# Optimization experiments

Hardware: AMD Instinct MI355X
Metric: run time of the kernel (lower is better)

## Reference

```python
import jax, jax.numpy as jnp
import numpy as np

DIM_Q = 512
DIM_K = 512
D_Q4 = float(DIM_Q) ** 0.25  # torch: dim_q ** (1/4)
D_K4 = float(DIM_K) ** 0.25


def setup_inputs() -> dict:
    key = jax.random.key(0)
    ks = jax.random.split(key, 9)
    B, N, D_IN = 8, 4096, 512
    s_in = 1.0 / np.sqrt(D_IN)
    return {
        "x_q": jax.random.normal(ks[0], (B, N, D_IN), jnp.float32),
        "x_k": jax.random.normal(ks[1], (B, N, D_IN), jnp.float32),
        "x_v": jax.random.normal(ks[2], (B, N, D_IN), jnp.float32),
        # Linear params stored as [in, out] for x @ W + b
        "W_q": jax.random.uniform(ks[3], (D_IN, DIM_Q), jnp.float32, -s_in, s_in),
        "b_q": jax.random.uniform(ks[4], (DIM_Q,), jnp.float32, -s_in, s_in),
        "W_k": jax.random.uniform(ks[5], (D_IN, DIM_K), jnp.float32, -s_in, s_in),
        "b_k": jax.random.uniform(ks[6], (DIM_K,), jnp.float32, -s_in, s_in),
        "W_v": jax.random.uniform(ks[7], (D_IN, DIM_K), jnp.float32, -s_in, s_in),
        "b_v": jax.random.uniform(ks[8], (DIM_K,), jnp.float32, -s_in, s_in),
    }


def reference(x_q, x_k, x_v, W_q, b_q, W_k, b_k, W_v, b_v):
    Q = x_q @ W_q + b_q          # [B, n, dq]
    K = x_k @ W_k + b_k          # [B, n, dk]
    V = x_v @ W_v + b_v          # [B, n, dk]
    # softmax_row: over sequence axis (dim=-2) of Q
    A = jax.nn.softmax(Q / D_Q4, axis=-2)          # [B, n, dq]
    # softmax_col on K^T (dim=-1) == softmax over sequence axis of K
    Ks = jax.nn.softmax(K / D_K4, axis=-2)         # [B, n, dk]
    Bm = jnp.einsum("bnd,bne->bde", Ks, V)        # [B, dk, dk]
    Z = jnp.einsum("bnd,bde->bne", A, Bm)         # [B, n, dk]
    return Z
```

## Files before the change

### kernel.cpp

```cpp
#include <hip/hip_runtime.h>
#include <hip/hip_bf16.h>


typedef __bf16 bf16_t;
typedef __attribute__((ext_vector_type(8))) __bf16 bf16x8;
typedef __attribute__((ext_vector_type(4))) __bf16 bf16x4;
typedef __attribute__((ext_vector_type(4))) float f32x4;

#define MFMA_BF16 __builtin_amdgcn_mfma_f32_16x16x32_bf16

__device__ inline void async_ld16(const void* g, void* l) {
  __builtin_amdgcn_global_load_lds(
      (const __attribute__((address_space(1))) void*)g,
      (__attribute__((address_space(3))) void*)l, 16, 0, 0);
}

#define INV_D4 0.2102241038134287f

#define BAR_LGKM()                                        \
  do {                                                    \
    asm volatile("s_waitcnt lgkmcnt(0)" ::: "memory");    \
    __builtin_amdgcn_s_barrier();                         \
  } while (0)

#define BAR_VM_LGKM()                                             \
  do {                                                            \
    asm volatile("s_waitcnt vmcnt(0) lgkmcnt(0)" ::: "memory");   \
    __builtin_amdgcn_s_barrier();                                 \
  } while (0)

__device__ inline void cvt_store4(bf16_t* dst, const float4* f, int cch,
                                  int xr, int half) {
#pragma unroll
  for (int i = 0; i < 4; ++i) {
    bf16x4 v;
    v[0] = (__bf16)f[i].x; v[1] = (__bf16)f[i].y;
    v[2] = (__bf16)f[i].z; v[3] = (__bf16)f[i].w;
    *(bf16x4*)(dst + (size_t)(cch * 132 + xr + 32 * i) * 8 + half * 4) = v;
  }
}

__global__ __launch_bounds__(256) void wt_kernel(
    const float* __restrict__ Wq, const float* __restrict__ Wk,
    const float* __restrict__ Wv, bf16_t* __restrict__ Wt) {
  const int z = blockIdx.z;
  const float* W = (z == 0) ? Wq : (z == 1) ? Wk : Wv;
  bf16_t* O = Wt + (size_t)z * 262144;
  __shared__ __align__(16) bf16_t tile[64 * 72];
  const int t = threadIdx.x;
  const int r = t >> 2;
  const int c4 = (t & 3) * 16;
  const int in0 = blockIdx.x * 64, out0 = blockIdx.y * 64;
  const float* src = W + (size_t)(in0 + r) * 512 + out0 + c4;
#pragma unroll
  for (int i = 0; i < 4; ++i) {
    float4 f = ((const float4*)src)[i];
    tile[(c4 + i * 4 + 0) * 72 + r] = (__bf16)f.x;
    tile[(c4 + i * 4 + 1) * 72 + r] = (__bf16)f.y;
    tile[(c4 + i * 4 + 2) * 72 + r] = (__bf16)f.z;
    tile[(c4 + i * 4 + 3) * 72 + r] = (__bf16)f.w;
  }
  __syncthreads();
  bf16x8* dst = (bf16x8*)(O + (size_t)(out0 + r) * 512 + in0 + c4);
  const bf16x8* s = (const bf16x8*)(tile + r * 72 + c4);
  dst[0] = s[0];
  dst[1] = s[1];
}

__global__ __launch_bounds__(256, 2) void proj_q(
    const float* __restrict__ Xq, const bf16_t* __restrict__ Wt,
    const float* __restrict__ bias, bf16_t* __restrict__ Eq,
    float* __restrict__ Sq) {
  __shared__ __align__(16) bf16_t Xs[2][4224];

  const int t = threadIdx.x;
  const int lane = t & 63, w = t >> 6;
  const int quad = lane >> 4, l15 = lane & 15;
  const int m0 = blockIdx.x * 128;
  const int n0 = blockIdx.y * 256 + w * 64;

  f32x4 acc[8][4];
  const f32x4 zero4 = {0.f, 0.f, 0.f, 0.f};
#pragma unroll
  for (int i = 0; i < 8; ++i)
#pragma unroll
    for (int j = 0; j < 4; ++j) acc[i][j] = zero4;

  const int xr = t >> 3;
  const int f4 = t & 7;
  const int cch = f4 >> 1, half = f4 & 1;
  const float* abase = Xq + (size_t)(m0 + xr) * 512 + f4 * 4;
  const bf16_t* wbase = Wt + (size_t)(n0 + l15) * 512 + quad * 8;

  float4 fb[2][4];
  bf16x8 wr[2][4];

#pragma unroll
  for (int i = 0; i < 4; ++i) fb[1][i] = *(const float4*)(abase + i * 16384);
#pragma unroll
  for (int ni = 0; ni < 4; ++ni)
    wr[0][ni] = *(const bf16x8*)(wbase + ni * 8192);
#pragma unroll
  for (int i = 0; i < 4; ++i)
    fb[0][i] = *(const float4*)(abase + i * 16384 + 32);
  cvt_store4(Xs[0], fb[1], cch, xr, half);
#pragma unroll
  for (int i = 0; i < 4; ++i)
    fb[1][i] = *(const float4*)(abase + i * 16384 + 64);
  BAR_LGKM();

#pragma unroll
  for (int ks = 0; ks < 16; ++ks) {
    const int p = ks & 1;
    bf16x8 af[8];
#pragma unroll
    for (int mi = 0; mi < 8; ++mi)
      af[mi] = *(const bf16x8*)(&Xs[p][(size_t)(quad * 132 + mi * 16 + l15) * 8]);
    if (ks < 15) {
      cvt_store4(Xs[p ^ 1], fb[p], cch, xr, half);
#pragma unroll
      for (int ni = 0; ni < 4; ++ni)
        wr[p ^ 1][ni] = *(const bf16x8*)(wbase + ni * 8192 + (ks + 1) * 32);
      if (ks < 13) {
#pragma unroll
        for (int i = 0; i < 4; ++i)
          fb[p][i] = *(const float4*)(abase + i * 16384 + (ks + 3) * 32);
      }
    }
#pragma unroll
    for (int mi = 0; mi < 8; ++mi)
#pragma unroll
      for (int ni = 0; ni < 4; ++ni)
        acc[mi][ni] = MFMA_BF16(af[mi], wr[p][ni], acc[mi][ni], 0, 0, 0);
    if (ks < 15) BAR_LGKM();
  }

  const int b = m0 >> 12;
  float cs[4] = {0.f, 0.f, 0.f, 0.f};
#pragma unroll
  for (int ni = 0; ni < 4; ++ni) {
    const int col = n0 + ni * 16 + l15;
    const float bv_ = bias[col];
#pragma unroll
    for (int mi = 0; mi < 8; ++mi)
#pragma unroll
      for (int r = 0; r < 4; ++r) {
        const int row = m0 + mi * 16 + quad * 4 + r;
        float v = __expf((acc[mi][ni][r] + bv_) * INV_D4);
        Eq[(size_t)row * 512 + col] = (bf16_t)v;
        cs[ni] += v;
      }
  }
#pragma unroll
  for (int ni = 0; ni < 4; ++ni) {
    cs[ni] += __shfl_xor(cs[ni], 16);
    cs[ni] += __shfl_xor(cs[ni], 32);
  }
  if (lane < 16) {
#pragma unroll
    for (int ni = 0; ni < 4; ++ni)
      atomicAdd(&Sq[b * 512 + n0 + ni * 16 + lane], cs[ni]);
  }
}

__global__ __launch_bounds__(256, 2) void proj_kv(
    const float* __restrict__ xk, const float* __restrict__ xv,
    const bf16_t* __restrict__ Wt, const float* __restrict__ bk,
    const float* __restrict__ bv, bf16_t* __restrict__ Ft,
    bf16_t* __restrict__ Vt) {
  const int z = blockIdx.z + 1;
  const float* X = (z == 1) ? xk : xv;
  const float* bias = (z == 1) ? bk : bv;
  const bf16_t* W = Wt + (size_t)z * 262144;
  bf16_t* Out = (z == 1) ? Ft : Vt;
  const bool expm = (z == 1);

  __shared__ __align__(16) bf16_t Xs[2][4224];

  const int t = threadIdx.x;
  const int lane = t & 63, w = t >> 6;
  const int quad = lane >> 4, l15 = lane & 15;
  const int ng = blockIdx.x * 128;
  const int d0 = blockIdx.y * 256 + w * 64;

  f32x4 acc[4][8];
  const f32x4 zero4 = {0.f, 0.f, 0.f, 0.f};
#pragma unroll
  for (int i = 0; i < 4; ++i)
#pragma unroll
    for (int j = 0; j < 8; ++j) acc[i][j] = zero4;

  const int xr = t >> 3;
  const int f4 = t & 7;
  const int cch = f4 >> 1, half = f4 & 1;
  const float* bbase = X + (size_t)(ng + xr) * 512 + f4 * 4;
  const bf16_t* wbase = W + (size_t)(d0 + l15) * 512 + quad * 8;

  float4 fb[2][4];
  bf16x8 wr[2][4];

#pragma unroll
  for (int i = 0; i < 4; ++i) fb[1][i] = *(const float4*)(bbase + i * 16384);
#pragma unroll
  for (int mi = 0; mi < 4; ++mi)
    wr[0][mi] = *(const bf16x8*)(wbase + mi * 8192);
#pragma unroll
  for (int i = 0; i < 4; ++i)
    fb[0][i] = *(const float4*)(bbase + i * 16384 + 32);
  cvt_store4(Xs[0], fb[1], cch, xr, half);
#pragma unroll
  for (int i = 0; i < 4; ++i)
    fb[1][i] = *(const float4*)(bbase + i * 16384 + 64);
  BAR_LGKM();

#pragma unroll
  for (int ks = 0; ks < 16; ++ks) {
    const int p = ks & 1;
    bf16x8 bx[8];
#pragma unroll
    for (int ni = 0; ni < 8; ++ni)
      bx[ni] = *(const bf16x8*)(&Xs[p][(size_t)(quad * 132 + ni * 16 + l15) * 8]);
    if (ks < 15) {
      cvt_store4(Xs[p ^ 1], fb[p], cch, xr, half);
#pragma unroll
      for (int mi = 0; mi < 4; ++mi)
        wr[p ^ 1][mi] = *(const bf16x8*)(wbase + mi * 8192 + (ks + 1) * 32);
      if (ks < 13) {
#pragma unroll
        for (int i = 0; i < 4; ++i)
          fb[p][i] = *(const float4*)(bbase + i * 16384 + (ks + 3) * 32);
      }
    }
#pragma unroll
    for (int mi = 0; mi < 4; ++mi)
#pragma unroll
      for (int ni = 0; ni < 8; ++ni)
        acc[mi][ni] = MFMA_BF16(wr[p][mi], bx[ni], acc[mi][ni], 0, 0, 0);
    if (ks < 15) BAR_LGKM();
  }

  const int b = ng >> 12;
  const int nl0 = (ng & 4095);
#pragma unroll
  for (int mi = 0; mi < 4; ++mi)
#pragma unroll
    for (int r = 0; r < 4; ++r) {
      const int d = d0 + mi * 16 + quad * 4 + r;
      const float bv_ = bias[d];
      bf16_t* rowp = Out + (size_t)b * 2097152 + (size_t)d * 4096 + nl0;
#pragma unroll
      for (int ni = 0; ni < 8; ++ni) {
        float v = acc[mi][ni][r] + bv_;
        if (expm) v = __expf(v * INV_D4);
        rowp[ni * 16 + l15] = (bf16_t)v;
      }
    }
}

__global__ __launch_bounds__(256) void sk_kernel(const bf16_t* __restrict__ Ft,
                                                 float* __restrict__ Sk) {
  const int row = blockIdx.x * 4 + (threadIdx.x >> 6);
  const int lane = threadIdx.x & 63;
  const bf16x8* p = (const bf16x8*)(Ft + (size_t)row * 4096) + lane;
  float s = 0.f;
#pragma unroll
  for (int j = 0; j < 8; ++j) {
    bf16x8 v = p[j * 64];
#pragma unroll
    for (int e = 0; e < 8; ++e) s += (float)v[e];
  }
#pragma unroll
  for (int m = 1; m <= 32; m <<= 1) s += __shfl_xor(s, m);
  if (lane == 0) Sk[row] = s;
}

__global__ __launch_bounds__(256, 2) void bm_gemm(
    const bf16_t* __restrict__ Ft, const bf16_t* __restrict__ Vt,
    float* __restrict__ Bmp, int S) {
  const int b = blockIdx.z / S;
  const int s = blockIdx.z - b * S;
  const int d0 = blockIdx.x * 128;
  const int e0 = blockIdx.y * 128;
  const bf16_t* A = Ft + (size_t)b * 2097152;
  const bf16_t* B = Vt + (size_t)b * 2097152;
  float* out = Bmp + ((size_t)s * 8 + b) * 262144;

  __shared__ __align__(16) bf16_t As[2][8192];
  __shared__ __align__(16) bf16_t Bs[2][8192];

  const int t = threadIdx.x;
  const int lane = t & 63, w = t >> 6;
  const int quad = lane >> 4, l15 = lane & 15;
  const int m_off = (w & 1) * 64, n_off = (w >> 1) * 64;

  const int kper = 4096 / S;
  const int KS = kper >> 6;
  const int kbase = s * kper;

  f32x4 acc[4][4];
  const f32x4 zero4 = {0.f, 0.f, 0.f, 0.f};
#pragma unroll
  for (int i = 0; i < 4; ++i)
#pragma unroll
    for (int j = 0; j < 4; ++j) acc[i][j] = zero4;

  const int srow = lane >> 3;
  const int spiece = (lane & 7) ^ srow;
  const bf16_t* asrc = A + (size_t)(d0 + srow) * 4096 + kbase + spiece * 8;
  const bf16_t* bsrc = B + (size_t)(e0 + srow) * 4096 + kbase + spiece * 8;
  const int q0 = w * 4;
  const int rsw = l15 & 7;

  auto stage = [&](int buf, int ks) {
#pragma unroll
    for (int i = 0; i < 4; ++i) {
      const int q = q0 + i;
      async_ld16(asrc + (size_t)q * 8 * 4096 + ks * 64, &As[buf][q * 512]);
      async_ld16(bsrc + (size_t)q * 8 * 4096 + ks * 64, &Bs[buf][q * 512]);
    }
  };

  stage(0, 0);
  BAR_VM_LGKM();

  for (int ks = 0; ks < KS; ++ks) {
    const int p = ks & 1;
    if (ks + 1 < KS) stage(p ^ 1, ks + 1);
#pragma unroll
    for (int ksub = 0; ksub < 2; ++ksub) {
      const int c = ksub * 4 + quad;
      bf16x8 af[4], bfr[4];
#pragma unroll
      for (int mi = 0; mi < 4; ++mi) {
        const int row = m_off + mi * 16 + l15;
        af[mi] = *(const bf16x8*)(&As[p][(size_t)row * 64 + ((c ^ rsw) << 3)]);
      }
#pragma unroll
      for (int ni = 0; ni < 4; ++ni) {
        const int row = n_off + ni * 16 + l15;
        bfr[ni] = *(const bf16x8*)(&Bs[p][(size_t)row * 64 + ((c ^ rsw) << 3)]);
      }
#pragma unroll
      for (int mi = 0; mi < 4; ++mi)
#pragma unroll
        for (int ni = 0; ni < 4; ++ni)
          acc[mi][ni] = MFMA_BF16(af[mi], bfr[ni], acc[mi][ni], 0, 0, 0);
    }
    if (ks + 1 < KS) BAR_VM_LGKM();
  }

#pragma unroll
  for (int mi = 0; mi < 4; ++mi)
#pragma unroll
    for (int ni = 0; ni < 4; ++ni) {
      const int ecol = e0 + n_off + ni * 16 + l15;
#pragma unroll
      for (int r = 0; r < 4; ++r) {
        const int drow = d0 + m_off + mi * 16 + quad * 4 + r;
        out[(size_t)drow * 512 + ecol] = acc[mi][ni][r];
      }
    }
}

__global__ __launch_bounds__(256) void scale_kernel(
    const float* __restrict__ Bmp, const float* __restrict__ Sq,
    const float* __restrict__ Sk, bf16_t* __restrict__ Ct, int S) {
  const int b = blockIdx.z;
  const int d0 = blockIdx.x * 64, e0 = blockIdx.y * 64;
  __shared__ __align__(16) bf16_t tile[64 * 72];
  const int t = threadIdx.x;
  const int r = t >> 2;
  const int c4 = (t & 3) * 16;
  const int d = d0 + r;
  const float f = 1.0f / (Sq[b * 512 + d] * Sk[b * 512 + d]);
  const float* p0 = Bmp + (size_t)b * 262144 + (size_t)d * 512 + e0 + c4;
#pragma unroll
  for (int i = 0; i < 4; ++i) {
    float sx = 0.f, sy = 0.f, sz = 0.f, sw = 0.f;
    for (int sp = 0; sp < S; ++sp) {
      float4 v = ((const float4*)(p0 + (size_t)sp * 2097152))[i];
      sx += v.x; sy += v.y; sz += v.z; sw += v.w;
    }
    tile[(c4 + i * 4 + 0) * 72 + r] = (__bf16)(sx * f);
    tile[(c4 + i * 4 + 1) * 72 + r] = (__bf16)(sy * f);
    tile[(c4 + i * 4 + 2) * 72 + r] = (__bf16)(sz * f);
    tile[(c4 + i * 4 + 3) * 72 + r] = (__bf16)(sw * f);
  }
  __syncthreads();
  bf16x8* dst = (bf16x8*)(Ct + (size_t)b * 262144 + (size_t)(e0 + r) * 512 + d0 + c4);
  const bf16x8* sptr = (const bf16x8*)(tile + r * 72 + c4);
  dst[0] = sptr[0];
  dst[1] = sptr[1];
}

__global__ __launch_bounds__(256, 2) void z_gemm(
    const bf16_t* __restrict__ Eq, const bf16_t* __restrict__ Ct,
    float* __restrict__ out) {
  __shared__ __align__(16) bf16_t As[2][8192];

  const int t = threadIdx.x;
  const int lane = t & 63, w = t >> 6;
  const int quad = lane >> 4, l15 = lane & 15;
  const int m0 = blockIdx.x * 128;
  const int n0 = blockIdx.y * 256 + w * 64;
  const int batch = m0 >> 12;
  const bf16_t* Bt = Ct + (size_t)batch * 262144;

  f32x4 acc[8][4];
  const f32x4 zero4 = {0.f, 0.f, 0.f, 0.f};
#pragma unroll
  for (int i = 0; i < 8; ++i)
#pragma unroll
    for (int j = 0; j < 4; ++j) acc[i][j] = zero4;

  const int srow = lane >> 3;
  const int spiece = (lane & 7) ^ srow;
  const bf16_t* asrc = Eq + (size_t)(m0 + srow) * 512 + spiece * 8;
  const int q0 = w * 4;
  const int rsw = l15 & 7;
  const bf16_t* wbase = Bt + (size_t)(n0 + l15) * 512 + quad * 8;

  auto stageZ = [&](int buf, int ks) {
#pragma unroll
    for (int i = 0; i < 4; ++i) {
      const int q = q0 + i;
      async_ld16(asrc + (size_t)q * 8 * 512 + ks * 64, &As[buf][q * 512]);
    }
  };

  stageZ(0, 0);
  BAR_VM_LGKM();

#pragma unroll
  for (int ks = 0; ks < 8; ++ks) {
    const int p = ks & 1;
    if (ks < 7) stageZ(p ^ 1, ks + 1);
    bf16x8 wrA[4], wrB[4];
#pragma unroll
    for (int ni = 0; ni < 4; ++ni) {
      wrA[ni] = *(const bf16x8*)(wbase + ni * 8192 + ks * 64);
      wrB[ni] = *(const bf16x8*)(wbase + ni * 8192 + ks * 64 + 32);
    }
#pragma unroll
    for (int ksub = 0; ksub < 2; ++ksub) {
      const int c = ksub * 4 + quad;
      bf16x8 af[8];
#pragma unroll
      for (int mi = 0; mi < 8; ++mi) {
        const int row = mi * 16 + l15;
        af[mi] = *(const bf16x8*)(&As[p][(size_t)row * 64 + ((c ^ rsw) << 3)]);
      }
#pragma unroll
      for (int mi = 0; mi < 8; ++mi)
#pragma unroll
        for (int ni = 0; ni < 4; ++ni)
          acc[mi][ni] =
              MFMA_BF16(af[mi], ksub ? wrB[ni] : wrA[ni], acc[mi][ni], 0, 0, 0);
    }
    if (ks < 7) BAR_VM_LGKM();
  }

#pragma unroll
  for (int mi = 0; mi < 8; ++mi)
#pragma unroll
    for (int ni = 0; ni < 4; ++ni) {
      const int col = n0 + ni * 16 + l15;
#pragma unroll
      for (int r = 0; r < 4; ++r) {
        const int row = m0 + mi * 16 + quad * 4 + r;
        out[(size_t)row * 512 + col] = acc[mi][ni][r];
      }
    }
}

extern "C" void kernel_launch(void* const* d_in, const int* in_sizes, int n_in,
                              void* d_out, int out_size, void* d_ws,
                              size_t ws_size, hipStream_t stream) {
  const float* xq = (const float*)d_in[0];
  const float* xk = (const float*)d_in[1];
  const float* xv = (const float*)d_in[2];
  const float* Wq = (const float*)d_in[3];
  const float* bq = (const float*)d_in[4];
  const float* Wk = (const float*)d_in[5];
  const float* bk = (const float*)d_in[6];
  const float* Wv = (const float*)d_in[7];
  const float* bv = (const float*)d_in[8];
  float* out = (float*)d_out;

  char* ws = (char*)d_ws;
  bf16_t* Eq = (bf16_t*)(ws + 0);
  bf16_t* Ft = (bf16_t*)(ws + 33554432);
  bf16_t* Vt = (bf16_t*)(ws + 67108864);
  float* Bmp = (float*)(ws + 100663296);

  const int S = (ws_size >= (size_t)135823360) ? 4 : 2;
  const size_t wt_off = (S == 4) ? (size_t)134217728 : (size_t)117440512;
  bf16_t* Wt = (bf16_t*)(ws + wt_off);
  float* Sq = (float*)(ws + wt_off + 1572864);
  float* Sk = (float*)(ws + wt_off + 1572864 + 16384);
  bf16_t* Ct = (bf16_t*)(ws + 33554432);

  hipMemsetAsync(Sq, 0, 16384, stream);

  wt_kernel<<<dim3(8, 8, 3), 256, 0, stream>>>(Wq, Wk, Wv, Wt);
  proj_q<<<dim3(256, 2), 256, 0, stream>>>(xq, Wt, bq, Eq, Sq);
  proj_kv<<<dim3(256, 2, 2), 256, 0, stream>>>(xk, xv, Wt, bk, bv, Ft, Vt);
  sk_kernel<<<dim3(1024), 256, 0, stream>>>(Ft, Sk);
  bm_gemm<<<dim3(4, 4, 8 * S), 256, 0, stream>>>(Ft, Vt, Bmp, S);
  scale_kernel<<<dim3(8, 8, 8), 256, 0, stream>>>(Bmp, Sq, Sk, Ct, S);
  z_gemm<<<dim3(256, 2), 256, 0, stream>>>(Eq, Ct, out);
}
```

Before: 357.2 us.

## Stage fp32 X tiles via async global-to-LDS loads with swizzle in projections

```diff
diff --git a/kernel.cpp b/kernel.cpp
--- a/kernel.cpp
+++ b/kernel.cpp
@@ -16,12 +16,6 @@
 }
 
 #define INV_D4 0.2102241038134287f
-
-#define BAR_LGKM()                                        \
-  do {                                                    \
-    asm volatile("s_waitcnt lgkmcnt(0)" ::: "memory");    \
-    __builtin_amdgcn_s_barrier();                         \
-  } while (0)
 
 #define BAR_VM_LGKM()                                             \
   do {                                                            \
@@ -29,15 +23,29 @@
     __builtin_amdgcn_s_barrier();                                 \
   } while (0)
 
-__device__ inline void cvt_store4(bf16_t* dst, const float4* f, int cch,
-                                  int xr, int half) {
-#pragma unroll
-  for (int i = 0; i < 4; ++i) {
-    bf16x4 v;
-    v[0] = (__bf16)f[i].x; v[1] = (__bf16)f[i].y;
-    v[2] = (__bf16)f[i].z; v[3] = (__bf16)f[i].w;
-    *(bf16x4*)(dst + (size_t)(cch * 132 + xr + 32 * i) * 8 + half * 4) = v;
-  }
+#define BAR_VM8_LGKM()                                            \
+  do {                                                            \
+    asm volatile("s_waitcnt vmcnt(8) lgkmcnt(0)" ::: "memory");   \
+    __builtin_amdgcn_s_barrier();                                 \
+  } while (0)
+
+#define STAGE_X(LBUF, KS)                                                  \
+  _Pragma("unroll") for (int i_ = 0; i_ < 8; ++i_) {                       \
+    const int rw_ = w * 32 + i_ * 4 + (lane >> 4);                         \
+    const int pc_ = (lane & 15) ^ (rw_ & 15);                              \
+    async_ld16(Xb + (size_t)rw_ * 512 + (KS) * 64 + pc_ * 4,               \
+               (char*)(LBUF) + (w * 32 + i_ * 4) * 256);                   \
+  }
+
+__device__ inline bf16x8 frag_cvt(const float* lbuf, int row, int p0) {
+  const char* base = (const char*)lbuf + row * 256;
+  const int s = row & 15;
+  f32x4 a = *(const f32x4*)(base + (((p0 + 0) ^ s) << 4));
+  f32x4 b = *(const f32x4*)(base + (((p0 + 1) ^ s) << 4));
+  bf16x8 r;
+  r[0] = (__bf16)a[0]; r[1] = (__bf16)a[1]; r[2] = (__bf16)a[2]; r[3] = (__bf16)a[3];
+  r[4] = (__bf16)b[0]; r[5] = (__bf16)b[1]; r[6] = (__bf16)b[2]; r[7] = (__bf16)b[3];
+  return r;
 }
 
 __global__ __launch_bounds__(256) void wt_kernel(
@@ -71,81 +79,74 @@
     const float* __restrict__ Xq, const bf16_t* __restrict__ Wt,
     const float* __restrict__ bias, bf16_t* __restrict__ Eq,
     float* __restrict__ Sq) {
-  __shared__ __align__(16) bf16_t Xs[2][4224];
+  __shared__ __align__(16) float Xf[2][8192];
 
   const int t = threadIdx.x;
   const int lane = t & 63, w = t >> 6;
   const int quad = lane >> 4, l15 = lane & 15;
   const int m0 = blockIdx.x * 128;
-  const int n0 = blockIdx.y * 256 + w * 64;
-
-  f32x4 acc[8][4];
+  const int n0 = blockIdx.y * 128;
+  const int m_off = (w & 1) * 64, n_off = (w >> 1) * 64;
+
+  f32x4 acc[4][4];
   const f32x4 zero4 = {0.f, 0.f, 0.f, 0.f};
 #pragma unroll
-  for (int i = 0; i < 8; ++i)
+  for (int i = 0; i < 4; ++i)
 #pragma unroll
     for (int j = 0; j < 4; ++j) acc[i][j] = zero4;
 
-  const int xr = t >> 3;
-  const int f4 = t & 7;
-  const int cch = f4 >> 1, half = f4 & 1;
-  const float* abase = Xq + (size_t)(m0 + xr) * 512 + f4 * 4;
-  const bf16_t* wbase = Wt + (size_t)(n0 + l15) * 512 + quad * 8;
-
-  float4 fb[2][4];
-  bf16x8 wr[2][4];
-
-#pragma unroll
-  for (int i = 0; i < 4; ++i) fb[1][i] = *(const float4*)(abase + i * 16384);
-#pragma unroll
-  for (int ni = 0; ni < 4; ++ni)
-    wr[0][ni] = *(const bf16x8*)(wbase + ni * 8192);
-#pragma unroll
-  for (int i = 0; i < 4; ++i)
-    fb[0][i] = *(const float4*)(abase + i * 16384 + 32);
-  cvt_store4(Xs[0], fb[1], cch, xr, half);
-#pragma unroll
-  for (int i = 0; i < 4; ++i)
-    fb[1][i] = *(const float4*)(abase + i * 16384 + 64);
-  BAR_LGKM();
-
-#pragma unroll
-  for (int ks = 0; ks < 16; ++ks) {
-    const int p = ks & 1;
-    bf16x8 af[8];
-#pragma unroll
-    for (int mi = 0; mi < 8; ++mi)
-      af[mi] = *(const bf16x8*)(&Xs[p][(size_t)(quad * 132 + mi * 16 + l15) * 8]);
-    if (ks < 15) {
-      cvt_store4(Xs[p ^ 1], fb[p], cch, xr, half);
-#pragma unroll
-      for (int ni = 0; ni < 4; ++ni)
-        wr[p ^ 1][ni] = *(const bf16x8*)(wbase + ni * 8192 + (ks + 1) * 32);
-      if (ks < 13) {
-#pragma unroll
-        for (int i = 0; i < 4; ++i)
-          fb[p][i] = *(const float4*)(abase + i * 16384 + (ks + 3) * 32);
-      }
-    }
-#pragma unroll
-    for (int mi = 0; mi < 8; ++mi)
-#pragma unroll
-      for (int ni = 0; ni < 4; ++ni)
-        acc[mi][ni] = MFMA_BF16(af[mi], wr[p][ni], acc[mi][ni], 0, 0, 0);
-    if (ks < 15) BAR_LGKM();
-  }
+  const float* Xb = Xq + (size_t)m0 * 512;
+  const bf16_t* wbase = Wt + (size_t)(n0 + n_off + l15) * 512 + quad * 8;
+
+  bf16x8 wA[4][2], wB[4][2];
+
+#define Q_LOAD_W(WBUF, KS)                                                 \
+  _Pragma("unroll") for (int ni_ = 0; ni_ < 4; ++ni_)                      \
+    _Pragma("unroll") for (int u_ = 0; u_ < 2; ++u_)                       \
+      WBUF[ni_][u_] =                                                      \
+          *(const bf16x8*)(wbase + ni_ * 8192 + (KS) * 64 + u_ * 32);
+
+#define Q_STEP(KS, CUR, NXT, WC, WN, FULL)                                 \
+  {                                                                        \
+    if (FULL) {                                                            \
+      STAGE_X(NXT, (KS) + 1);                                              \
+      asm volatile("" ::: "memory");                                       \
+      Q_LOAD_W(WN, (KS) + 1);                                              \
+    }                                                                      \
+    _Pragma("unroll") for (int u = 0; u < 2; ++u)                          \
+      _Pragma("unroll") for (int mi = 0; mi < 4; ++mi) {                   \
+        bf16x8 ax = frag_cvt(CUR, m_off + mi * 16 + l15, u * 8 + quad * 2);\
+        _Pragma("unroll") for (int ni = 0; ni < 4; ++ni)                   \
+          acc[mi][ni] = MFMA_BF16(ax, WC[ni][u], acc[mi][ni], 0, 0, 0);    \
+      }                                                                    \
+    if (FULL) BAR_VM8_LGKM();                                              \
+  }
+
+  STAGE_X(Xf[0], 0);
+  asm volatile("" ::: "memory");
+  Q_LOAD_W(wA, 0);
+  BAR_VM8_LGKM();
+
+  Q_STEP(0, Xf[0], Xf[1], wA, wB, true);
+  Q_STEP(1, Xf[1], Xf[0], wB, wA, true);
+  Q_STEP(2, Xf[0], Xf[1], wA, wB, true);
+  Q_STEP(3, Xf[1], Xf[0], wB, wA, true);
+  Q_STEP(4, Xf[0], Xf[1], wA, wB, true);
+  Q_STEP(5, Xf[1], Xf[0], wB, wA, true);
+  Q_STEP(6, Xf[0], Xf[1], wA, wB, true);
+  Q_STEP(7, Xf[1], Xf[0], wB, wA, false);
 
   const int b = m0 >> 12;
   float cs[4] = {0.f, 0.f, 0.f, 0.f};
 #pragma unroll
   for (int ni = 0; ni < 4; ++ni) {
-    const int col = n0 + ni * 16 + l15;
+    const int col = n0 + n_off + ni * 16 + l15;
     const float bv_ = bias[col];
 #pragma unroll
-    for (int mi = 0; mi < 8; ++mi)
+    for (int mi = 0; mi < 4; ++mi)
 #pragma unroll
       for (int r = 0; r < 4; ++r) {
-        const int row = m0 + mi * 16 + quad * 4 + r;
+        const int row = m0 + m_off + mi * 16 + quad * 4 + r;
         float v = __expf((acc[mi][ni][r] + bv_) * INV_D4);
         Eq[(size_t)row * 512 + col] = (bf16_t)v;
         cs[ni] += v;
@@ -159,8 +160,10 @@
   if (lane < 16) {
 #pragma unroll
     for (int ni = 0; ni < 4; ++ni)
-      atomicAdd(&Sq[b * 512 + n0 + ni * 16 + lane], cs[ni]);
-  }
+      atomicAdd(&Sq[b * 512 + n0 + n_off + ni * 16 + lane], cs[ni]);
+  }
+#undef Q_STEP
+#undef Q_LOAD_W
 }
 
 __global__ __launch_bounds__(256, 2) void proj_kv(
@@ -175,86 +178,81 @@
   bf16_t* Out = (z == 1) ? Ft : Vt;
   const bool expm = (z == 1);
 
-  __shared__ __align__(16) bf16_t Xs[2][4224];
+  __shared__ __align__(16) float Xf[2][8192];
 
   const int t = threadIdx.x;
   const int lane = t & 63, w = t >> 6;
   const int quad = lane >> 4, l15 = lane & 15;
   const int ng = blockIdx.x * 128;
-  const int d0 = blockIdx.y * 256 + w * 64;
-
-  f32x4 acc[4][8];
+  const int d0 = blockIdx.y * 128;
+  const int d_off = (w & 1) * 64, n_off = (w >> 1) * 64;
+
+  f32x4 acc[4][4];
   const f32x4 zero4 = {0.f, 0.f, 0.f, 0.f};
 #pragma unroll
   for (int i = 0; i < 4; ++i)
 #pragma unroll
-    for (int j = 0; j < 8; ++j) acc[i][j] = zero4;
-
-  const int xr = t >> 3;
-  const int f4 = t & 7;
-  const int cch = f4 >> 1, half = f4 & 1;
-  const float* bbase = X + (size_t)(ng + xr) * 512 + f4 * 4;
-  const bf16_t* wbase = W + (size_t)(d0 + l15) * 512 + quad * 8;
-
-  float4 fb[2][4];
-  bf16x8 wr[2][4];
-
-#pragma unroll
-  for (int i = 0; i < 4; ++i) fb[1][i] = *(const float4*)(bbase + i * 16384);
+    for (int j = 0; j < 4; ++j) acc[i][j] = zero4;
+
+  const float* Xb = X + (size_t)ng * 512;
+  const bf16_t* wbase = W + (size_t)(d0 + d_off + l15) * 512 + quad * 8;
+
+  bf16x8 wA[4][2], wB[4][2];
+
+#define KV_LOAD_W(WBUF, KS)                                                \
+  _Pragma("unroll") for (int mi_ = 0; mi_ < 4; ++mi_)                      \
+    _Pragma("unroll") for (int u_ = 0; u_ < 2; ++u_)                       \
+      WBUF[mi_][u_] =                                                      \
+          *(const bf16x8*)(wbase + mi_ * 8192 + (KS) * 64 + u_ * 32);
+
+#define KV_STEP(KS, CUR, NXT, WC, WN, FULL)                                \
+  {                                                                        \
+    if (FULL) {                                                            \
+      STAGE_X(NXT, (KS) + 1);                                              \
+      asm volatile("" ::: "memory");                                       \
+      KV_LOAD_W(WN, (KS) + 1);                                             \
+    }                                                                      \
+    _Pragma("unroll") for (int u = 0; u < 2; ++u)                          \
+      _Pragma("unroll") for (int ni = 0; ni < 4; ++ni) {                   \
+        bf16x8 bx = frag_cvt(CUR, n_off + ni * 16 + l15, u * 8 + quad * 2);\
+        _Pragma("unroll") for (int mi = 0; mi < 4; ++mi)                   \
+          acc[mi][ni] = MFMA_BF16(WC[mi][u], bx, acc[mi][ni], 0, 0, 0);    \
+      }                                                                    \
+    if (FULL) BAR_VM8_LGKM();                                              \
+  }
+
+  STAGE_X(Xf[0], 0);
+  asm volatile("" ::: "memory");
+  KV_LOAD_W(wA, 0);
+  BAR_VM8_LGKM();
+
+  KV_STEP(0, Xf[0], Xf[1], wA, wB, true);
+  KV_STEP(1, Xf[1], Xf[0], wB, wA, true);
+  KV_STEP(2, Xf[0], Xf[1], wA, wB, true);
+  KV_STEP(3, Xf[1], Xf[0], wB, wA, true);
+  KV_STEP(4, Xf[0], Xf[1], wA, wB, true);
+  KV_STEP(5, Xf[1], Xf[0], wB, wA, true);
+  KV_STEP(6, Xf[0], Xf[1], wA, wB, true);
+  KV_STEP(7, Xf[1], Xf[0], wB, wA, false);
+
+  const int b = ng >> 12;
+  const int nl0 = (ng & 4095) + n_off;
 #pragma unroll
   for (int mi = 0; mi < 4; ++mi)
-    wr[0][mi] = *(const bf16x8*)(wbase + mi * 8192);
-#pragma unroll
-  for (int i = 0; i < 4; ++i)
-    fb[0][i] = *(const float4*)(bbase + i * 16384 + 32);
-  cvt_store4(Xs[0], fb[1], cch, xr, half);
-#pragma unroll
-  for (int i = 0; i < 4; ++i)
-    fb[1][i] = *(const float4*)(bbase + i * 16384 + 64);
-  BAR_LGKM();
-
-#pragma unroll
-  for (int ks = 0; ks < 16; ++ks) {
-    const int p = ks & 1;
-    bf16x8 bx[8];
-#pragma unroll
-    for (int ni = 0; ni < 8; ++ni)
-      bx[ni] = *(const bf16x8*)(&Xs[p][(size_t)(quad * 132 + ni * 16 + l15) * 8]);
-    if (ks < 15) {
-      cvt_store4(Xs[p ^ 1], fb[p], cch, xr, half);
-#pragma unroll
-      for (int mi = 0; mi < 4; ++mi)
-        wr[p ^ 1][mi] = *(const bf16x8*)(wbase + mi * 8192 + (ks + 1) * 32);
-      if (ks < 13) {
-#pragma unroll
-        for (int i = 0; i < 4; ++i)
-          fb[p][i] = *(const float4*)(bbase + i * 16384 + (ks + 3) * 32);
-      }
-    }
-#pragma unroll
-    for (int mi = 0; mi < 4; ++mi)
-#pragma unroll
-      for (int ni = 0; ni < 8; ++ni)
-        acc[mi][ni] = MFMA_BF16(wr[p][mi], bx[ni], acc[mi][ni], 0, 0, 0);
-    if (ks < 15) BAR_LGKM();
-  }
-
-  const int b = ng >> 12;
-  const int nl0 = (ng & 4095);
-#pragma unroll
-  for (int mi = 0; mi < 4; ++mi)
 #pragma unroll
     for (int r = 0; r < 4; ++r) {
-      const int d = d0 + mi * 16 + quad * 4 + r;
+      const int d = d0 + d_off + mi * 16 + quad * 4 + r;
       const float bv_ = bias[d];
       bf16_t* rowp = Out + (size_t)b * 2097152 + (size_t)d * 4096 + nl0;
 #pragma unroll
-      for (int ni = 0; ni < 8; ++ni) {
+      for (int ni = 0; ni < 4; ++ni) {
         float v = acc[mi][ni][r] + bv_;
         if (expm) v = __expf(v * INV_D4);
         rowp[ni * 16 + l15] = (bf16_t)v;
       }
     }
+#undef KV_STEP
+#undef KV_LOAD_W
 }
 
 __global__ __launch_bounds__(256) void sk_kernel(const bf16_t* __restrict__ Ft,
@@ -503,8 +501,8 @@
   hipMemsetAsync(Sq, 0, 16384, stream);
 
   wt_kernel<<<dim3(8, 8, 3), 256, 0, stream>>>(Wq, Wk, Wv, Wt);
-  proj_q<<<dim3(256, 2), 256, 0, stream>>>(xq, Wt, bq, Eq, Sq);
-  proj_kv<<<dim3(256, 2, 2), 256, 0, stream>>>(xk, xv, Wt, bk, bv, Ft, Vt);
+  proj_q<<<dim3(256, 4), 256, 0, stream>>>(xq, Wt, bq, Eq, Sq);
+  proj_kv<<<dim3(256, 4, 2), 256, 0, stream>>>(xk, xv, Wt, bk, bv, Ft, Vt);
   sk_kernel<<<dim3(1024), 256, 0, stream>>>(Ft, Sk);
   bm_gemm<<<dim3(4, 4, 8 * S), 256, 0, stream>>>(Ft, Vt, Bmp, S);
   scale_kernel<<<dim3(8, 8, 8), 256, 0, stream>>>(Bmp, Sq, Sk, Ct, S);
```

New measurement: 409.8 us. 1.15x slower.
